# Kernel optimization log

Measured on AMD Instinct MI355X. Metric: run time of the kernel, lower is better.

## Reference

```python
import jax, jax.numpy as jnp
import numpy as np

N_TASK = 50000
N_PROC = 256
N_EDGES = 800000
EMB = 64
HEADS = 4
NLAYERS = 3
EDIM = 8
TDIM = 16
PDIM = 8
NGRAPHS = 8


def setup_inputs():
    key = jax.random.key(0)
    ks = jax.random.split(key, 30)

    def nrm(k, shape, fan_in):
        return jax.random.normal(k, shape, jnp.float32) / np.float32(np.sqrt(fan_in))

    inp = {}
    inp["x_task"] = jax.random.normal(ks[0], (N_TASK, TDIM), jnp.float32)
    inp["x_proc"] = jax.random.normal(ks[1], (N_PROC, PDIM), jnp.float32)
    inp["edge_index"] = jax.random.randint(ks[2], (2, N_EDGES), 0, N_TASK, dtype=jnp.int32)
    inp["edge_attr"] = jax.random.uniform(ks[3], (N_EDGES, EDIM), jnp.float32)
    inp["task_batch"] = jnp.sort(jax.random.randint(ks[4], (N_TASK,), 0, NGRAPHS, dtype=jnp.int32))
    inp["proc_batch"] = jnp.sort(jax.random.randint(ks[5], (N_PROC,), 0, NGRAPHS, dtype=jnp.int32))
    # input embeds
    inp["W_task"] = nrm(ks[6], (TDIM, EMB), TDIM)
    inp["b_task"] = jnp.zeros((EMB,), jnp.float32)
    inp["W_proc"] = nrm(ks[7], (PDIM, EMB), PDIM)
    inp["b_proc"] = jnp.zeros((EMB,), jnp.float32)
    # per-layer GAT params (stacked over layers)
    inp["gat_W"] = nrm(ks[8], (NLAYERS, EMB, HEADS * EMB), EMB)
    inp["gat_We"] = nrm(ks[9], (NLAYERS, EDIM, HEADS * EMB), EDIM)
    inp["att_src"] = nrm(ks[10], (NLAYERS, HEADS, EMB), EMB)
    inp["att_dst"] = nrm(ks[11], (NLAYERS, HEADS, EMB), EMB)
    inp["att_edge"] = nrm(ks[12], (NLAYERS, HEADS, EMB), EMB)
    inp["gat_b"] = jnp.zeros((NLAYERS, HEADS * EMB), jnp.float32)
    inp["proj_W"] = nrm(ks[13], (NLAYERS, HEADS * EMB, EMB), HEADS * EMB)
    inp["proj_b"] = jnp.zeros((NLAYERS, EMB), jnp.float32)
    inp["ln_g"] = jnp.ones((NLAYERS, EMB), jnp.float32)
    inp["ln_b"] = jnp.zeros((NLAYERS, EMB), jnp.float32)
    # heads
    inp["pt_W1"] = nrm(ks[14], (EMB, EMB // 2), EMB)
    inp["pt_b1"] = jnp.zeros((EMB // 2,), jnp.float32)
    inp["pt_W2"] = nrm(ks[15], (EMB // 2, 1), EMB // 2)
    inp["pt_b2"] = jnp.zeros((1,), jnp.float32)
    inp["v_W1"] = nrm(ks[16], (2 * EMB, EMB), 2 * EMB)
    inp["v_b1"] = jnp.zeros((EMB,), jnp.float32)
    inp["v_W2"] = nrm(ks[17], (EMB, 1), EMB)
    inp["v_b2"] = jnp.zeros((1,), jnp.float32)
    return inp


def _gat_layer(x, src, dst, eattr, W, We, a_s, a_d, a_e, bias):
    # PyG GATConv(in=-1 shared lin, heads=H, concat=True, edge_dim) with self loops already appended
    n = x.shape[0]
    xl = (x @ W).reshape(n, HEADS, EMB)            # [N,H,D]
    el = (eattr @ We).reshape(-1, HEADS, EMB)      # [E,H,D]
    a_src = jnp.einsum("nhd,hd->nh", xl, a_s)
    a_dst = jnp.einsum("nhd,hd->nh", xl, a_d)
    a_edg = jnp.einsum("ehd,hd->eh", el, a_e)
    alpha = jax.nn.leaky_relu(a_src[src] + a_dst[dst] + a_edg, 0.2)  # [E,H]
    m = jax.ops.segment_max(alpha, dst, num_segments=n)
    ex = jnp.exp(alpha - m[dst])
    denom = jax.ops.segment_sum(ex, dst, num_segments=n)
    coeff = ex / (denom[dst] + 1e-16)
    out = jax.ops.segment_sum(coeff[:, :, None] * xl[src], dst, num_segments=n)
    return out.reshape(n, HEADS * EMB) + bias


def _mean_pool(x, batch, g):
    s = jax.ops.segment_sum(x, batch, num_segments=g)
    cnt = jax.ops.segment_sum(jnp.ones((x.shape[0], 1), x.dtype), batch, num_segments=g)
    return s / jnp.maximum(cnt, 1.0)


def reference(x_task, x_proc, edge_attr, W_task, b_task, W_proc, b_proc, gat_W, gat_We,
              att_src, att_dst, att_edge, gat_b, proj_W, proj_b, ln_g, ln_b,
              pt_W1, pt_b1, pt_W2, pt_b2, v_W1, v_b1, v_W2, v_b2,
              edge_index, task_batch, proc_batch):
    h_t = x_task @ W_task + b_task
    h_p = x_proc @ W_proc + b_proc
    # add self loops; self-loop edge_attr = mean of edge_attr (PyG fill_value='mean')
    loop = jnp.arange(N_TASK, dtype=edge_index.dtype)
    src = jnp.concatenate([edge_index[0], loop])
    dst = jnp.concatenate([edge_index[1], loop])
    ea = jnp.concatenate([edge_attr, jnp.broadcast_to(edge_attr.mean(0), (N_TASK, EDIM))], axis=0)
    for l in range(NLAYERS):
        upd = _gat_layer(h_t, src, dst, ea, gat_W[l], gat_We[l], att_src[l], att_dst[l], att_edge[l], gat_b[l])
        upd = jax.nn.elu(upd @ proj_W[l] + proj_b[l])
        h = h_t + upd
        mu = h.mean(-1, keepdims=True)
        var = ((h - mu) ** 2).mean(-1, keepdims=True)
        h_t = (h - mu) / jnp.sqrt(var + 1e-5) * ln_g[l] + ln_b[l]
    task_logits = (jax.nn.relu(h_t @ pt_W1 + pt_b1) @ pt_W2 + pt_b2)[:, 0]
    tp = _mean_pool(h_t, task_batch, NGRAPHS)
    pp = _mean_pool(h_p, proc_batch, NGRAPHS)
    ge = jnp.concatenate([tp, pp], axis=1)
    value = jax.nn.relu(ge @ v_W1 + v_b1) @ v_W2 + v_b2
    return task_logits, value, h_t, h_p
```

## Files before the change

### kernel.cpp

```cpp
#include <hip/hip_runtime.h>
#include <hip/hip_bf16.h>
#include <math.h>

#define NT 50000
#define NP 256
#define NE 800000
#define ET 850000
#define EMBD 64
#define NHEADS 4
#define HE 256
#define NG 8
#define NBLK 49

typedef __attribute__((ext_vector_type(8))) short bf16x8;
typedef __attribute__((ext_vector_type(4))) float f32x4;

#define OFF_DEG    0u
#define OFF_INDPTR 200192u
#define OFF_CURSOR 400384u
#define OFF_BLKSUM 600576u
#define OFF_MG     600832u
#define OFF_MH     601216u
#define OFF_MEAN   601280u
#define OFF_TPSUM  601344u
#define OFF_TPCNT  603392u
#define OFF_ER     603648u
#define OFF_ASRC   7403648u
#define OFF_ADST   8204416u
#define OFF_HT     9005184u
#define OFF_HTB    21817472u
#define OFF_XL     28223616u
#define OFF_AGG    53823616u
#define OFF_WXF    79448192u
#define OFF_WPF    79546496u

__device__ __forceinline__ float bf_lo(unsigned int u) {
  union { unsigned int i; float f; } v; v.i = u << 16; return v.f;
}
__device__ __forceinline__ float bf_hi(unsigned int u) {
  union { unsigned int i; float f; } v; v.i = u & 0xffff0000u; return v.f;
}

__global__ __launch_bounds__(256) void k_embed_task(const float* __restrict__ x,
    const float* __restrict__ W, const float* __restrict__ b,
    float* __restrict__ ht, __hip_bfloat16* __restrict__ htb) {
  int lane = threadIdx.x & 63, wid = threadIdx.x >> 6;
  float breg[16];
  #pragma unroll
  for (int k = 0; k < 16; k++) breg[k] = W[k * 64 + lane];
  float bias = b[lane];
  int row0 = blockIdx.x * 64 + wid * 16;
  #pragma unroll 1
  for (int r = 0; r < 16; r++) {
    int row = row0 + r;
    if (row >= NT) return;
    const float4* xr = (const float4*)(x + (size_t)row * 16);
    float acc = bias;
    #pragma unroll
    for (int q = 0; q < 4; q++) {
      float4 v = xr[q];
      acc += v.x * breg[q*4+0] + v.y * breg[q*4+1] + v.z * breg[q*4+2] + v.w * breg[q*4+3];
    }
    ht[(size_t)row * 64 + lane] = acc;
    htb[(size_t)row * 64 + lane] = __float2bfloat16(acc);
  }
}

__global__ __launch_bounds__(256) void k_degree_mean(const int* __restrict__ ei1,
    const float* __restrict__ ea, int* __restrict__ deg, float* __restrict__ sums) {
  __shared__ float lds[256];
  int tid = threadIdx.x;
  int e = blockIdx.x * 256 + tid;
  if (e < ET) {
    int d = (e < NE) ? ei1[e] : (e - NE);
    atomicAdd(&deg[d], 1);
  }
  int k = tid & 7, rl = tid >> 3;
  float s = 0.f;
  for (int row = blockIdx.x * 32 + rl; row < NE; row += gridDim.x * 32)
    s += ea[(size_t)row * 8 + k];
  lds[tid] = s;
  __syncthreads();
  for (int off = 128; off >= 8; off >>= 1) {
    if (tid < off) lds[tid] += lds[tid + off];
    __syncthreads();
  }
  if (tid < 8) atomicAdd(&sums[tid], lds[tid]);
}

__global__ __launch_bounds__(1024) void k_scanA(const int* __restrict__ deg,
    int* __restrict__ indptr, int* __restrict__ blksum) {
  __shared__ int wsum[16];
  int tid = threadIdx.x, lane = tid & 63, wid = tid >> 6;
  int i = blockIdx.x * 1024 + tid;
  int v = (i < NT) ? deg[i] : 0;
  int x = v;
  #pragma unroll
  for (int off = 1; off < 64; off <<= 1) {
    int t = __shfl_up(x, off, 64);
    if (lane >= off) x += t;
  }
  if (lane == 63) wsum[wid] = x;
  __syncthreads();
  if (wid == 0 && lane < 16) {
    int w = wsum[lane];
    #pragma unroll
    for (int off = 1; off < 16; off <<= 1) {
      int t = __shfl_up(w, off, 64);
      if (lane >= off) w += t;
    }
    wsum[lane] = w;
  }
  __syncthreads();
  int woff = (wid == 0) ? 0 : wsum[wid - 1];
  if (i < NT) indptr[i] = x + woff - v;
  if (tid == 1023) blksum[blockIdx.x] = wsum[15];
}

__global__ __launch_bounds__(1024) void k_scanB(const int* __restrict__ blksum,
    int* __restrict__ indptr, int* __restrict__ cursor) {
  __shared__ int bs[NBLK];
  int tid = threadIdx.x;
  if (tid < NBLK) bs[tid] = blksum[tid];
  __syncthreads();
  int off = 0;
  for (int j = 0; j < (int)blockIdx.x; j++) off += bs[j];
  int i = blockIdx.x * 1024 + tid;
  if (i < NT) {
    int e = indptr[i] + off;
    indptr[i] = e;
    cursor[i] = e;
  }
  if (blockIdx.x == 0 && tid == 0) {
    int tot = 0;
    for (int j = 0; j < NBLK; j++) tot += bs[j];
    indptr[NT] = tot;
  }
}

__global__ __launch_bounds__(256) void k_fill(const int* __restrict__ ei0,
                                              const int* __restrict__ ei1,
                                              int* __restrict__ cursor,
                                              uint2* __restrict__ er) {
  int e = blockIdx.x * 256 + threadIdx.x;
  if (e >= ET) return;
  int d, s;
  if (e < NE) { d = ei1[e]; s = ei0[e]; } else { d = e - NE; s = e - NE; }
  int p = atomicAdd(&cursor[d], 1);
  uint2 r; r.x = (unsigned)e; r.y = (unsigned)s;
  er[p] = r;
}

__global__ __launch_bounds__(128) void k_mprep(const float* __restrict__ We,
    const float* __restrict__ ae, const float* __restrict__ msum,
    float* __restrict__ Mg, float* __restrict__ Mh) {
  int t = threadIdx.x;
  if (t < 96) {
    int l = t >> 5, idx = t & 31, k = idx >> 2, h = idx & 3;
    const float* Wl = We + (size_t)l * 8 * HE;
    const float* al = ae + (size_t)l * NHEADS * EMBD;
    float s = 0.f;
    #pragma unroll
    for (int d = 0; d < 64; d++) s += Wl[k * HE + h * 64 + d] * al[h * 64 + d];
    Mg[t] = s;
  }
  __syncthreads();
  if (t < 12) {
    int l = t >> 2, h = t & 3;
    float m = 0.f;
    #pragma unroll
    for (int k = 0; k < 8; k++) m += msum[k] * (1.f / NE) * Mg[l * 32 + k * 4 + h];
    Mh[t] = m;
  }
}

__global__ void k_prep_w(const float* __restrict__ Wx, const float* __restrict__ Wp,
                         __hip_bfloat16* __restrict__ Wxf, __hip_bfloat16* __restrict__ Wpf) {
  int lane = threadIdx.x;
  int bid = blockIdx.x;
  int quad = lane >> 4, l15 = lane & 15;
  if (bid < 96) {
    int l = bid >> 5, rem = bid & 31, t = rem >> 1, kb = rem & 1;
    const float* Wl = Wx + (size_t)l * 64 * 256;
    __hip_bfloat16* out = Wxf + (size_t)l * 16384 + (size_t)((t * 2 + kb) * 64 + lane) * 8;
    #pragma unroll
    for (int j = 0; j < 8; j++)
      out[j] = __float2bfloat16(Wl[(kb * 32 + quad * 8 + j) * 256 + t * 16 + l15]);
  } else {
    bid -= 96;
    int l = bid >> 5, rem = bid & 31, t = rem >> 3, kb = rem & 7;
    const float* Wl = Wp + (size_t)l * 256 * 64;
    __hip_bfloat16* out = Wpf + (size_t)l * 16384 + (size_t)((t * 8 + kb) * 64 + lane) * 8;
    #pragma unroll
    for (int j = 0; j < 8; j++)
      out[j] = __float2bfloat16(Wl[(kb * 32 + quad * 8 + j) * 64 + t * 16 + l15]);
  }
}

__global__ __launch_bounds__(256) void k_xl_mfma(
    const __hip_bfloat16* __restrict__ htb, const __hip_bfloat16* __restrict__ Wf,
    const float* __restrict__ as, const float* __restrict__ ad,
    __hip_bfloat16* __restrict__ xl, float* __restrict__ a_src, float* __restrict__ a_dst) {
  int lane = threadIdx.x & 63, wave = threadIdx.x >> 6;
  int quad = lane >> 4, l15 = lane & 15;
  int r0 = blockIdx.x * 64 + wave * 16;
  f32x4 acc[16];
  #pragma unroll
  for (int t = 0; t < 16; t++) acc[t] = (f32x4){0.f, 0.f, 0.f, 0.f};
  #pragma unroll
  for (int kb = 0; kb < 2; kb++) {
    bf16x8 a = *(const bf16x8*)(htb + (size_t)(r0 + l15) * 64 + kb * 32 + quad * 8);
    #pragma unroll
    for (int t = 0; t < 16; t++) {
      bf16x8 bfr = *(const bf16x8*)(Wf + (size_t)((t * 2 + kb) * 64 + lane) * 8);
      acc[t] = __builtin_amdgcn_mfma_f32_16x16x32_bf16(a, bfr, acc[t], 0, 0, 0);
    }
  }
  float asv[16], adv[16];
  #pragma unroll
  for (int t = 0; t < 16; t++) { asv[t] = as[t * 16 + l15]; adv[t] = ad[t * 16 + l15]; }
  #pragma unroll
  for (int reg = 0; reg < 4; reg++) {
    int row = r0 + quad * 4 + reg;
    bool ok = row < NT;
    float vs[4] = {0.f, 0.f, 0.f, 0.f}, vd[4] = {0.f, 0.f, 0.f, 0.f};
    #pragma unroll
    for (int t = 0; t < 16; t++) {
      float v = acc[t][reg];
      if (ok) xl[(size_t)row * HE + t * 16 + l15] = __float2bfloat16(v);
      vs[t >> 2] += v * asv[t];
      vd[t >> 2] += v * adv[t];
    }
    #pragma unroll
    for (int off = 8; off; off >>= 1) {
      #pragma unroll
      for (int h = 0; h < 4; h++) {
        vs[h] += __shfl_xor(vs[h], off, 64);
        vd[h] += __shfl_xor(vd[h], off, 64);
      }
    }
    if (ok && l15 == 0) {
      float4 s4; s4.x = vs[0]; s4.y = vs[1]; s4.z = vs[2]; s4.w = vs[3];
      float4 d4; d4.x = vd[0]; d4.y = vd[1]; d4.z = vd[2]; d4.w = vd[3];
      *(float4*)(a_src + (size_t)row * 4) = s4;
      *(float4*)(a_dst + (size_t)row * 4) = d4;
    }
  }
}

__global__ __launch_bounds__(256) void k_attn(
    const __hip_bfloat16* __restrict__ xl, const float* __restrict__ a_src,
    const float* __restrict__ a_dst, const float* __restrict__ ea,
    const uint2* __restrict__ er, const int* __restrict__ indptr,
    const float* __restrict__ Mg, const float* __restrict__ Mh,
    const float* __restrict__ gb, __hip_bfloat16* __restrict__ agg) {
  int node = blockIdx.x * 4 + (threadIdx.x >> 6);
  int lane = threadIdx.x & 63;
  int h = lane >> 4;
  int hbase = lane & 48;
  int e15 = lane & 15;
  float MsR[8];
  #pragma unroll
  for (int k = 0; k < 8; k++) MsR[k] = Mg[k * 4 + h];
  float mhR = Mh[h];
  int beg = indptr[node], end = indptr[node + 1];
  float adh = a_dst[node * 4 + h];
  float M = -1e30f, S = 0.f;
  float acc0 = 0.f, acc1 = 0.f, acc2 = 0.f, acc3 = 0.f;
  for (int base = beg; base < end; base += 16) {
    int cnt = min(16, end - base);
    int el = base + e15;
    bool ok = e15 < cnt;
    uint2 r = ok ? er[el] : (uint2){0u, 0u};
    int e = (int)r.x;
    int my_src = (int)r.y;
    float asr = ok ? a_src[(size_t)my_src * 4 + h] : 0.f;
    float aeh;
    if (e < NE) {
      const float4* p = (const float4*)(ea + (size_t)e * 8);
      float4 v0 = p[0], v1 = p[1];
      aeh = v0.x * MsR[0] + v0.y * MsR[1] + v0.z * MsR[2] + v0.w * MsR[3]
          + v1.x * MsR[4] + v1.y * MsR[5] + v1.z * MsR[6] + v1.w * MsR[7];
    } else {
      aeh = mhR;
    }
    float al = asr + adh + aeh;
    al = (al > 0.f) ? al : 0.2f * al;
    if (!ok) al = -1e30f;
    float cm = al;
    #pragma unroll
    for (int off = 1; off < 16; off <<= 1) cm = fmaxf(cm, __shfl_xor(cm, off, 64));
    float newM = fmaxf(M, cm);
    float corr = __expf(M - newM);
    float ex = __expf(al - newM);
    float cs = ex;
    #pragma unroll
    for (int off = 1; off < 16; off <<= 1) cs += __shfl_xor(cs, off, 64);
    S = S * corr + cs;
    M = newM;
    acc0 *= corr; acc1 *= corr; acc2 *= corr; acc3 *= corr;
    if (cnt == 16) {
      #pragma unroll 4
      for (int j = 0; j < 16; j++) {
        int src = __shfl(my_src, j, 64);
        float cf = __shfl(ex, hbase | j, 64);
        uint2 u = *(const uint2*)(xl + (size_t)src * HE + lane * 4);
        acc0 += cf * bf_lo(u.x);
        acc1 += cf * bf_hi(u.x);
        acc2 += cf * bf_lo(u.y);
        acc3 += cf * bf_hi(u.y);
      }
    } else {
      for (int j = 0; j < cnt; j++) {
        int src = __shfl(my_src, j, 64);
        float cf = __shfl(ex, hbase | j, 64);
        uint2 u = *(const uint2*)(xl + (size_t)src * HE + lane * 4);
        acc0 += cf * bf_lo(u.x);
        acc1 += cf * bf_hi(u.x);
        acc2 += cf * bf_lo(u.y);
        acc3 += cf * bf_hi(u.y);
      }
    }
  }
  float inv = 1.f / (S + 1e-16f);
  float4 g4 = *(const float4*)(gb + lane * 4);
  unsigned int o0 = __bfloat16_as_ushort(__float2bfloat16(acc0 * inv + g4.x));
  unsigned int o1 = __bfloat16_as_ushort(__float2bfloat16(acc1 * inv + g4.y));
  unsigned int o2 = __bfloat16_as_ushort(__float2bfloat16(acc2 * inv + g4.z));
  unsigned int o3 = __bfloat16_as_ushort(__float2bfloat16(acc3 * inv + g4.w));
  uint2 out; out.x = o0 | (o1 << 16); out.y = o2 | (o3 << 16);
  *(uint2*)(agg + (size_t)node * HE + lane * 4) = out;
}

__global__ __launch_bounds__(256) void k_proj_mfma(
    const __hip_bfloat16* __restrict__ agg, const __hip_bfloat16* __restrict__ Wf,
    const float* __restrict__ pb, const float* __restrict__ g, const float* __restrict__ b,
    const float* __restrict__ ht_in, float* __restrict__ ht_out,
    __hip_bfloat16* __restrict__ htb_out, int writebf) {
  int lane = threadIdx.x & 63, wave = threadIdx.x >> 6;
  int quad = lane >> 4, l15 = lane & 15;
  int r0 = blockIdx.x * 64 + wave * 16;
  f32x4 acc[4];
  #pragma unroll
  for (int t = 0; t < 4; t++) acc[t] = (f32x4){0.f, 0.f, 0.f, 0.f};
  #pragma unroll
  for (int kb = 0; kb < 8; kb++) {
    bf16x8 a = *(const bf16x8*)(agg + (size_t)(r0 + l15) * HE + kb * 32 + quad * 8);
    #pragma unroll
    for (int t = 0; t < 4; t++) {
      bf16x8 bfr = *(const bf16x8*)(Wf + (size_t)((t * 8 + kb) * 64 + lane) * 8);
      acc[t] = __builtin_amdgcn_mfma_f32_16x16x32_bf16(a, bfr, acc[t], 0, 0, 0);
    }
  }
  float pbv[4], gv[4], bv[4];
  #pragma unroll
  for (int t = 0; t < 4; t++) {
    pbv[t] = pb[t * 16 + l15];
    gv[t] = g[t * 16 + l15];
    bv[t] = b[t * 16 + l15];
  }
  #pragma unroll
  for (int reg = 0; reg < 4; reg++) {
    int row = r0 + quad * 4 + reg;
    bool ok = row < NT;
    float h[4], rs = 0.f;
    #pragma unroll
    for (int t = 0; t < 4; t++) {
      float u = acc[t][reg] + pbv[t];
      u = (u > 0.f) ? u : (__expf(u) - 1.f);
      h[t] = ht_in[(size_t)row * 64 + t * 16 + l15] + u;
      rs += h[t];
    }
    #pragma unroll
    for (int off = 8; off; off >>= 1) rs += __shfl_xor(rs, off, 64);
    float mu = rs * 0.015625f;
    float vv = 0.f;
    #pragma unroll
    for (int t = 0; t < 4; t++) { float d = h[t] - mu; vv += d * d; }
    #pragma unroll
    for (int off = 8; off; off >>= 1) vv += __shfl_xor(vv, off, 64);
    float rstd = rsqrtf(vv * 0.015625f + 1e-5f);
    #pragma unroll
    for (int t = 0; t < 4; t++) {
      float o = (h[t] - mu) * rstd * gv[t] + bv[t];
      if (ok) {
        ht_out[(size_t)row * 64 + t * 16 + l15] = o;
        if (writebf) htb_out[(size_t)row * 64 + t * 16 + l15] = __float2bfloat16(o);
      }
    }
  }
}

__global__ __launch_bounds__(256) void k_task_head(const float* __restrict__ ht,
    const float* __restrict__ W1, const float* __restrict__ b1,
    const float* __restrict__ W2, const float* __restrict__ b2, float* __restrict__ logits) {
  __shared__ float lh[8 * 64];
  int t = threadIdx.x;
  size_t base = (size_t)blockIdx.x * 8 * 64;
  lh[t] = ht[base + t];
  lh[t + 256] = ht[base + t + 256];
  __syncthreads();
  int i = t >> 5, j = t & 31;
  float s = b1[j];
  #pragma unroll 8
  for (int d = 0; d < 64; d++) s += lh[i * 64 + d] * W1[d * 32 + j];
  s = fmaxf(s, 0.f);
  float p = s * W2[j];
  #pragma unroll
  for (int off = 16; off; off >>= 1) p += __shfl_xor(p, off, 64);
  if (j == 0) logits[blockIdx.x * 8 + i] = p + b2[0];
}

__global__ __launch_bounds__(256) void k_pool_task(const float* __restrict__ ht,
    const int* __restrict__ tb, float* __restrict__ sums, float* __restrict__ cnt) {
  int lane = threadIdx.x & 63, sub = threadIdx.x >> 6;
  float acc[8], c[8];
  #pragma unroll
  for (int g = 0; g < 8; g++) { acc[g] = 0.f; c[g] = 0.f; }
  int lim = min(NT, (int)((blockIdx.x + 1) * 512));
  for (int n = blockIdx.x * 512 + sub; n < lim; n += 4) {
    int g = tb[n];
    float v = ht[(size_t)n * 64 + lane];
    #pragma unroll
    for (int gg = 0; gg < 8; gg++) {
      if (g == gg) { acc[gg] += v; c[gg] += 1.f; }
    }
  }
  #pragma unroll
  for (int g = 0; g < 8; g++) {
    if (__any(acc[g] != 0.f || c[g] != 0.f)) {
      atomicAdd(&sums[g * 64 + lane], acc[g]);
      if (lane == 0) atomicAdd(&cnt[g], c[g]);
    }
  }
}

__global__ __launch_bounds__(512) void k_value(const float* __restrict__ tpsum,
    const float* __restrict__ tpcnt, const float* __restrict__ x_proc,
    const float* __restrict__ W_proc, const float* __restrict__ b_proc,
    float* __restrict__ hp_out, const int* __restrict__ pbatch,
    const float* __restrict__ vW1, const float* __restrict__ vb1,
    const float* __restrict__ vW2, const float* __restrict__ vb2,
    float* __restrict__ val_out) {
  __shared__ float ge[8 * 128];
  int t = threadIdx.x;
  int g = t >> 6, d = t & 63;
  float wreg[8];
  #pragma unroll
  for (int k = 0; k < 8; k++) wreg[k] = W_proc[k * 64 + d];
  float bd = b_proc[d];
  for (int p = g; p < 256; p += 8) {
    const float* xr = x_proc + (size_t)p * 8;
    float a = bd;
    #pragma unroll
    for (int k = 0; k < 8; k++) a += xr[k] * wreg[k];
    hp_out[(size_t)p * 64 + d] = a;
  }
  __syncthreads();
  float c = fmaxf(tpcnt[g], 1.f);
  ge[g * 128 + d] = tpsum[g * 64 + d] / c;
  float s = 0.f, cc = 0.f;
  for (int p = 0; p < 256; p++) {
    int bg = pbatch[p];
    if (bg == g) { s += hp_out[(size_t)p * 64 + d]; cc += 1.f; }
  }
  ge[g * 128 + 64 + d] = s / fmaxf(cc, 1.f);
  __syncthreads();
  float acc = vb1[d];
  #pragma unroll 8
  for (int k = 0; k < 128; k++) acc += ge[g * 128 + k] * vW1[k * 64 + d];
  acc = fmaxf(acc, 0.f);
  float p = acc * vW2[d];
  #pragma unroll
  for (int off = 32; off; off >>= 1) p += __shfl_xor(p, off, 64);
  if (d == 0) val_out[g] = p + vb2[0];
}

extern "C" void kernel_launch(void* const* d_in, const int* in_sizes, int n_in,
                              void* d_out, int out_size, void* d_ws, size_t ws_size,
                              hipStream_t stream) {
  (void)in_sizes; (void)n_in; (void)out_size; (void)ws_size;
  const float* x_task  = (const float*)d_in[0];
  const float* x_proc  = (const float*)d_in[1];
  const int*   eidx    = (const int*)d_in[2];
  const float* eattr   = (const float*)d_in[3];
  const int*   tbatch  = (const int*)d_in[4];
  const int*   pbatch  = (const int*)d_in[5];
  const float* W_task  = (const float*)d_in[6];
  const float* b_task  = (const float*)d_in[7];
  const float* W_proc  = (const float*)d_in[8];
  const float* b_proc  = (const float*)d_in[9];
  const float* gat_W   = (const float*)d_in[10];
  const float* gat_We  = (const float*)d_in[11];
  const float* att_src = (const float*)d_in[12];
  const float* att_dst = (const float*)d_in[13];
  const float* att_edge= (const float*)d_in[14];
  const float* gat_b   = (const float*)d_in[15];
  const float* proj_W  = (const float*)d_in[16];
  const float* proj_b  = (const float*)d_in[17];
  const float* ln_g    = (const float*)d_in[18];
  const float* ln_b    = (const float*)d_in[19];
  const float* pt_W1   = (const float*)d_in[20];
  const float* pt_b1   = (const float*)d_in[21];
  const float* pt_W2   = (const float*)d_in[22];
  const float* pt_b2   = (const float*)d_in[23];
  const float* v_W1    = (const float*)d_in[24];
  const float* v_b1    = (const float*)d_in[25];
  const float* v_W2    = (const float*)d_in[26];
  const float* v_b2    = (const float*)d_in[27];

  char* ws = (char*)d_ws;
  int*   deg    = (int*)(ws + OFF_DEG);
  int*   indptr = (int*)(ws + OFF_INDPTR);
  int*   cursor = (int*)(ws + OFF_CURSOR);
  int*   blksum = (int*)(ws + OFF_BLKSUM);
  float* Mg     = (float*)(ws + OFF_MG);
  float* Mh     = (float*)(ws + OFF_MH);
  float* msum   = (float*)(ws + OFF_MEAN);
  float* tpsum  = (float*)(ws + OFF_TPSUM);
  float* tpcnt  = (float*)(ws + OFF_TPCNT);
  uint2* er     = (uint2*)(ws + OFF_ER);
  float* a_src  = (float*)(ws + OFF_ASRC);
  float* a_dst  = (float*)(ws + OFF_ADST);
  float* ht     = (float*)(ws + OFF_HT);
  __hip_bfloat16* htb = (__hip_bfloat16*)(ws + OFF_HTB);
  __hip_bfloat16* xl  = (__hip_bfloat16*)(ws + OFF_XL);
  __hip_bfloat16* agg = (__hip_bfloat16*)(ws + OFF_AGG);
  __hip_bfloat16* wxf = (__hip_bfloat16*)(ws + OFF_WXF);
  __hip_bfloat16* wpf = (__hip_bfloat16*)(ws + OFF_WPF);

  float* out_logits = (float*)d_out;
  float* out_value  = (float*)d_out + NT;
  float* out_ht     = (float*)d_out + NT + NG;
  float* out_hp     = (float*)d_out + NT + NG + (size_t)NT * EMBD;

  hipMemsetAsync(ws + OFF_DEG, 0, NT * 4, stream);
  hipMemsetAsync(ws + OFF_MEAN, 0, 2144, stream);

  k_embed_task<<<782, 256, 0, stream>>>(x_task, W_task, b_task, ht, htb);
  k_degree_mean<<<(ET + 255) / 256, 256, 0, stream>>>(eidx + NE, eattr, deg, msum);
  k_scanA<<<NBLK, 1024, 0, stream>>>(deg, indptr, blksum);
  k_scanB<<<NBLK, 1024, 0, stream>>>(blksum, indptr, cursor);
  k_mprep<<<1, 128, 0, stream>>>(gat_We, att_edge, msum, Mg, Mh);
  k_fill<<<(ET + 255) / 256, 256, 0, stream>>>(eidx, eidx + NE, cursor, er);
  k_prep_w<<<192, 64, 0, stream>>>(gat_W, proj_W, wxf, wpf);

  for (int l = 0; l < 3; l++) {
    k_xl_mfma<<<782, 256, 0, stream>>>(htb, wxf + (size_t)l * 16384,
                                       att_src + l * NHEADS * EMBD,
                                       att_dst + l * NHEADS * EMBD,
                                       xl, a_src, a_dst);
    k_attn<<<NT / 4, 256, 0, stream>>>(xl, a_src, a_dst, eattr, er, indptr,
                                       Mg + l * 32, Mh + l * 4,
                                       gat_b + l * HE, agg);
    float* htout = (l == 2) ? out_ht : ht;
    k_proj_mfma<<<782, 256, 0, stream>>>(agg, wpf + (size_t)l * 16384,
                                         proj_b + l * EMBD, ln_g + l * EMBD,
                                         ln_b + l * EMBD, ht, htout, htb,
                                         (l == 2) ? 0 : 1);
  }

  k_task_head<<<NT / 8, 256, 0, stream>>>(out_ht, pt_W1, pt_b1, pt_W2, pt_b2, out_logits);
  k_pool_task<<<(NT + 511) / 512, 256, 0, stream>>>(out_ht, tbatch, tpsum, tpcnt);
  k_value<<<1, 512, 0, stream>>>(tpsum, tpcnt, x_proc, W_proc, b_proc, out_hp,
                                 pbatch, v_W1, v_b1, v_W2, v_b2, out_value);
}
```

Measured before the change: 720.5 us.

## Precompute per-layer edge attention terms in CSR order during fill

The fill kernel now computes the edge-attribute attention contribution for all three layers and writes them, together with the source index, in CSR-sorted order. The attention kernel then reads one contiguous float per edge and head instead of gathering the 32-byte edge attribute row by original edge id and doing a dot product each layer. This removes scattered edge_attr reads from the three attention passes. In exchange the fill kernel does more work and writes about 40 MB of extra workspace.

Measured after the change: 719.8 us. No clear change (-0.1%).

```diff
diff --git a/kernel.cpp b/kernel.cpp
--- a/kernel.cpp
+++ b/kernel.cpp
@@ -24,15 +24,18 @@
 #define OFF_MEAN   601280u
 #define OFF_TPSUM  601344u
 #define OFF_TPCNT  603392u
-#define OFF_ER     603648u
-#define OFF_ASRC   7403648u
-#define OFF_ADST   8204416u
-#define OFF_HT     9005184u
-#define OFF_HTB    21817472u
-#define OFF_XL     28223616u
-#define OFF_AGG    53823616u
-#define OFF_WXF    79448192u
-#define OFF_WPF    79546496u
+#define OFF_SRCS   603648u
+#define OFF_AE0    4003648u
+#define OFF_AE1    17603648u
+#define OFF_AE2    31203648u
+#define OFF_ASRC   44803648u
+#define OFF_ADST   45604416u
+#define OFF_HT     46405184u
+#define OFF_HTB    59217472u
+#define OFF_XL     65623616u
+#define OFF_AGG    91223616u
+#define OFF_WXF    116848192u
+#define OFF_WPF    116946496u
 
 __device__ __forceinline__ float bf_lo(unsigned int u) {
   union { unsigned int i; float f; } v; v.i = u << 16; return v.f;
@@ -138,19 +141,6 @@
   }
 }
 
-__global__ __launch_bounds__(256) void k_fill(const int* __restrict__ ei0,
-                                              const int* __restrict__ ei1,
-                                              int* __restrict__ cursor,
-                                              uint2* __restrict__ er) {
-  int e = blockIdx.x * 256 + threadIdx.x;
-  if (e >= ET) return;
-  int d, s;
-  if (e < NE) { d = ei1[e]; s = ei0[e]; } else { d = e - NE; s = e - NE; }
-  int p = atomicAdd(&cursor[d], 1);
-  uint2 r; r.x = (unsigned)e; r.y = (unsigned)s;
-  er[p] = r;
-}
-
 __global__ __launch_bounds__(128) void k_mprep(const float* __restrict__ We,
     const float* __restrict__ ae, const float* __restrict__ msum,
     float* __restrict__ Mg, float* __restrict__ Mh) {
@@ -174,6 +164,53 @@
   }
 }
 
+__global__ __launch_bounds__(256) void k_fill(const int* __restrict__ ei0,
+    const int* __restrict__ ei1, const float* __restrict__ ea,
+    const float* __restrict__ Mg, const float* __restrict__ Mh,
+    int* __restrict__ cursor, int* __restrict__ srcs,
+    float4* __restrict__ ae0, float4* __restrict__ ae1, float4* __restrict__ ae2) {
+  __shared__ float MgS[96];
+  __shared__ float MhS[12];
+  int t = threadIdx.x;
+  if (t < 96) MgS[t] = Mg[t];
+  if (t < 12) MhS[t] = Mh[t];
+  __syncthreads();
+  int e = blockIdx.x * 256 + t;
+  if (e >= ET) return;
+  int d, s;
+  float4 r[3];
+  if (e < NE) {
+    d = ei1[e]; s = ei0[e];
+    const float4* pp = (const float4*)(ea + (size_t)e * 8);
+    float4 v0 = pp[0], v1 = pp[1];
+    float v[8] = {v0.x, v0.y, v0.z, v0.w, v1.x, v1.y, v1.z, v1.w};
+    #pragma unroll
+    for (int l = 0; l < 3; l++) {
+      float rr[4];
+      #pragma unroll
+      for (int h = 0; h < 4; h++) {
+        float acc = 0.f;
+        #pragma unroll
+        for (int k = 0; k < 8; k++) acc += v[k] * MgS[l * 32 + k * 4 + h];
+        rr[h] = acc;
+      }
+      r[l].x = rr[0]; r[l].y = rr[1]; r[l].z = rr[2]; r[l].w = rr[3];
+    }
+  } else {
+    d = e - NE; s = d;
+    #pragma unroll
+    for (int l = 0; l < 3; l++) {
+      r[l].x = MhS[l * 4 + 0]; r[l].y = MhS[l * 4 + 1];
+      r[l].z = MhS[l * 4 + 2]; r[l].w = MhS[l * 4 + 3];
+    }
+  }
+  int p = atomicAdd(&cursor[d], 1);
+  srcs[p] = s;
+  ae0[p] = r[0];
+  ae1[p] = r[1];
+  ae2[p] = r[2];
+}
+
 __global__ void k_prep_w(const float* __restrict__ Wx, const float* __restrict__ Wp,
                          __hip_bfloat16* __restrict__ Wxf, __hip_bfloat16* __restrict__ Wpf) {
   int lane = threadIdx.x;
@@ -250,19 +287,14 @@
 
 __global__ __launch_bounds__(256) void k_attn(
     const __hip_bfloat16* __restrict__ xl, const float* __restrict__ a_src,
-    const float* __restrict__ a_dst, const float* __restrict__ ea,
-    const uint2* __restrict__ er, const int* __restrict__ indptr,
-    const float* __restrict__ Mg, const float* __restrict__ Mh,
+    const float* __restrict__ a_dst, const float* __restrict__ aedg,
+    const int* __restrict__ indptr, const int* __restrict__ srcs,
     const float* __restrict__ gb, __hip_bfloat16* __restrict__ agg) {
   int node = blockIdx.x * 4 + (threadIdx.x >> 6);
   int lane = threadIdx.x & 63;
   int h = lane >> 4;
   int hbase = lane & 48;
   int e15 = lane & 15;
-  float MsR[8];
-  #pragma unroll
-  for (int k = 0; k < 8; k++) MsR[k] = Mg[k * 4 + h];
-  float mhR = Mh[h];
   int beg = indptr[node], end = indptr[node + 1];
   float adh = a_dst[node * 4 + h];
   float M = -1e30f, S = 0.f;
@@ -271,19 +303,9 @@
     int cnt = min(16, end - base);
     int el = base + e15;
     bool ok = e15 < cnt;
-    uint2 r = ok ? er[el] : (uint2){0u, 0u};
-    int e = (int)r.x;
-    int my_src = (int)r.y;
+    int my_src = ok ? srcs[el] : 0;
+    float aeh = ok ? aedg[(size_t)el * 4 + h] : 0.f;
     float asr = ok ? a_src[(size_t)my_src * 4 + h] : 0.f;
-    float aeh;
-    if (e < NE) {
-      const float4* p = (const float4*)(ea + (size_t)e * 8);
-      float4 v0 = p[0], v1 = p[1];
-      aeh = v0.x * MsR[0] + v0.y * MsR[1] + v0.z * MsR[2] + v0.w * MsR[3]
-          + v1.x * MsR[4] + v1.y * MsR[5] + v1.z * MsR[6] + v1.w * MsR[7];
-    } else {
-      aeh = mhR;
-    }
     float al = asr + adh + aeh;
     al = (al > 0.f) ? al : 0.2f * al;
     if (!ok) al = -1e30f;
@@ -519,7 +541,10 @@
   float* msum   = (float*)(ws + OFF_MEAN);
   float* tpsum  = (float*)(ws + OFF_TPSUM);
   float* tpcnt  = (float*)(ws + OFF_TPCNT);
-  uint2* er     = (uint2*)(ws + OFF_ER);
+  int*   srcs   = (int*)(ws + OFF_SRCS);
+  float4* ae0   = (float4*)(ws + OFF_AE0);
+  float4* ae1   = (float4*)(ws + OFF_AE1);
+  float4* ae2   = (float4*)(ws + OFF_AE2);
   float* a_src  = (float*)(ws + OFF_ASRC);
   float* a_dst  = (float*)(ws + OFF_ADST);
   float* ht     = (float*)(ws + OFF_HT);
@@ -528,6 +553,7 @@
   __hip_bfloat16* agg = (__hip_bfloat16*)(ws + OFF_AGG);
   __hip_bfloat16* wxf = (__hip_bfloat16*)(ws + OFF_WXF);
   __hip_bfloat16* wpf = (__hip_bfloat16*)(ws + OFF_WPF);
+  float* aedg[3] = {(float*)ae0, (float*)ae1, (float*)ae2};
 
   float* out_logits = (float*)d_out;
   float* out_value  = (float*)d_out + NT;
@@ -542,7 +568,8 @@
   k_scanA<<<NBLK, 1024, 0, stream>>>(deg, indptr, blksum);
   k_scanB<<<NBLK, 1024, 0, stream>>>(blksum, indptr, cursor);
   k_mprep<<<1, 128, 0, stream>>>(gat_We, att_edge, msum, Mg, Mh);
-  k_fill<<<(ET + 255) / 256, 256, 0, stream>>>(eidx, eidx + NE, cursor, er);
+  k_fill<<<(ET + 255) / 256, 256, 0, stream>>>(eidx, eidx + NE, eattr, Mg, Mh,
+                                               cursor, srcs, ae0, ae1, ae2);
   k_prep_w<<<192, 64, 0, stream>>>(gat_W, proj_W, wxf, wpf);
 
   for (int l = 0; l < 3; l++) {
@@ -550,8 +577,7 @@
                                        att_src + l * NHEADS * EMBD,
                                        att_dst + l * NHEADS * EMBD,
                                        xl, a_src, a_dst);
-    k_attn<<<NT / 4, 256, 0, stream>>>(xl, a_src, a_dst, eattr, er, indptr,
-                                       Mg + l * 32, Mh + l * 4,
+    k_attn<<<NT / 4, 256, 0, stream>>>(xl, a_src, a_dst, aedg[l], indptr, srcs,
                                        gat_b + l * HE, agg);
     float* htout = (l == 2) ? out_ht : ht;
     k_proj_mfma<<<782, 256, 0, stream>>>(agg, wpf + (size_t)l * 16384,
```
